# Kernel optimization log

Hardware: AMD Instinct MI355X
Metric: run time of the kernel (lower is better)

Reference implementation:

```python
import jax, jax.numpy as jnp
import numpy as np

EMBED_DIM = 1024
NUM_HEADS = 16
HEAD_DIM = EMBED_DIM // NUM_HEADS


def setup_inputs() -> dict:
    key = jax.random.key(0)
    kx, kq, kk, kv, ko = jax.random.split(key, 5)
    scale = 1.0 / np.sqrt(EMBED_DIM)
    return {
        "x": jax.random.normal(kx, (4, 2048, EMBED_DIM), dtype=jnp.float32),
        # nn.Linear weights are [out, in]; y = x @ W.T
        "w_q": jax.random.normal(kq, (EMBED_DIM, EMBED_DIM), dtype=jnp.float32) * scale,
        "w_k": jax.random.normal(kk, (EMBED_DIM, EMBED_DIM), dtype=jnp.float32) * scale,
        "w_v": jax.random.normal(kv, (EMBED_DIM, EMBED_DIM), dtype=jnp.float32) * scale,
        "w_o": jax.random.normal(ko, (EMBED_DIM, EMBED_DIM), dtype=jnp.float32) * scale,
    }


def reference(x, w_q, w_k, w_v, w_o):
    b, s, _ = x.shape
    # projections (Linear with no bias: x @ W.T)
    q = (x @ w_q.T).reshape(b, s, NUM_HEADS, HEAD_DIM).transpose(0, 2, 1, 3)
    k = (x @ w_k.T).reshape(b, s, NUM_HEADS, HEAD_DIM).transpose(0, 2, 1, 3)
    v = (x @ w_v.T).reshape(b, s, NUM_HEADS, HEAD_DIM).transpose(0, 2, 1, 3)
    # scores: [b, h, s, s]
    scores = jnp.einsum("bhqd,bhkd->bhqk", q, k) / jnp.sqrt(jnp.float32(HEAD_DIM)).astype(x.dtype)
    attn = jax.nn.softmax(scores, axis=-1)
    out = jnp.einsum("bhqk,bhkd->bhqd", attn, v)  # [b, h, s, d]
    out = out.transpose(0, 2, 1, 3).reshape(b, s, EMBED_DIM)
    return out @ w_o.T
```

## Files before the change

### kernel.cpp

```cpp
#include <hip/hip_runtime.h>
#include <math.h>

#define EMBED 1024
#define NHEAD 16
#define HDIM  64
#define BATCH 4
#define SEQ   2048
#define MROWS (BATCH * SEQ)

typedef __attribute__((ext_vector_type(8))) short short8;
typedef __attribute__((ext_vector_type(4))) float floatx4;
typedef __attribute__((ext_vector_type(16))) float floatx16;

#if __has_builtin(__builtin_amdgcn_exp2f)
#define EXP2(x) __builtin_amdgcn_exp2f(x)
#else
#define EXP2(x) exp2f(x)
#endif

__device__ __forceinline__ unsigned short f2bf(float f) {
  unsigned u = __float_as_uint(f);
  u += 0x7fffu + ((u >> 16) & 1u);
  return (unsigned short)(u >> 16);
}

#if __has_builtin(__builtin_amdgcn_cvt_pk_bf16_f32)
__device__ __forceinline__ unsigned pack2bf(float lo, float hi) {
  typedef __attribute__((ext_vector_type(2))) __bf16 bf2;
  union { bf2 b; unsigned u; } c;
  c.b = __builtin_amdgcn_cvt_pk_bf16_f32(lo, hi);
  return c.u;
}
#else
__device__ __forceinline__ unsigned pack2bf(float lo, float hi) {
  return ((__float_as_uint(lo) + 0x8000u) >> 16) |
         ((__float_as_uint(hi) + 0x8000u) & 0xffff0000u);
}
#endif

__device__ __forceinline__ void gl_lds16(const void* g, void* l) {
  __builtin_amdgcn_global_load_lds(
      (const __attribute__((address_space(1))) unsigned int*)g,
      (__attribute__((address_space(3))) unsigned int*)l, 16, 0, 0);
}

__global__ __launch_bounds__(256) void cast_bf16_kernel(
    const float* __restrict__ x,  const float* __restrict__ wq,
    const float* __restrict__ wk, const float* __restrict__ wv,
    const float* __restrict__ wo,
    unsigned short* __restrict__ xb, unsigned short* __restrict__ wb) {
  const size_t NX = (size_t)MROWS * EMBED;
  size_t i4 = ((size_t)blockIdx.x * 256 + threadIdx.x) * 4;
  const float* src;
  unsigned short* dst;
  size_t off;
  if (i4 < NX) {
    src = x; dst = xb; off = i4;
  } else {
    size_t j = i4 - NX;
    int r = (int)(j >> 20);
    off = j & ((1u << 20) - 1);
    src = (r == 0) ? wq : (r == 1) ? wk : (r == 2) ? wv : wo;
    dst = wb + ((size_t)r << 20);
  }
  float4 v = *(const float4*)(src + off);
  ushort4 o;
  o.x = f2bf(v.x); o.y = f2bf(v.y); o.z = f2bf(v.z); o.w = f2bf(v.w);
  *(ushort4*)(dst + off) = o;
}

__device__ __forceinline__ void gemm_core(
    const unsigned short* __restrict__ Amat,
    const unsigned short* __restrict__ Bmat,
    int mBase, int nBase,
    unsigned short* As, unsigned short* Bs,
    floatx4 acc[4][4]) {
  const int t = threadIdx.x;
  const int lane = t & 63, w = t >> 6;
  const int wr = w >> 1, wc = w & 1;
  const int quad = lane >> 4, l15 = lane & 15;

  const int f0 = (w * 2 + 0) * 64 + lane;
  const int f1 = (w * 2 + 1) * 64 + lane;
  const unsigned short* ga0 = Amat + (size_t)(mBase + (f0 >> 2)) * EMBED + (f0 & 3) * 8;
  const unsigned short* ga1 = Amat + (size_t)(mBase + (f1 >> 2)) * EMBED + (f1 & 3) * 8;
  const unsigned short* gb0 = Bmat + (size_t)(nBase + (f0 >> 2)) * EMBED + (f0 & 3) * 8;
  const unsigned short* gb1 = Bmat + (size_t)(nBase + (f1 >> 2)) * EMBED + (f1 & 3) * 8;
  unsigned short* la0 = As + (w * 2 + 0) * 512;
  unsigned short* la1 = As + (w * 2 + 1) * 512;
  unsigned short* lb0 = Bs + (w * 2 + 0) * 512;
  unsigned short* lb1 = Bs + (w * 2 + 1) * 512;

  for (int kb = 0; kb < EMBED; kb += 32) {
    __syncthreads();
    gl_lds16(ga0 + kb, la0);
    gl_lds16(ga1 + kb, la1);
    gl_lds16(gb0 + kb, lb0);
    gl_lds16(gb1 + kb, lb1);
    __syncthreads();
    short8 a[4], b[4];
#pragma unroll
    for (int mi = 0; mi < 4; ++mi)
      a[mi] = *(const short8*)&As[(wr * 64 + mi * 16 + l15) * 32 + quad * 8];
#pragma unroll
    for (int ni = 0; ni < 4; ++ni)
      b[ni] = *(const short8*)&Bs[(wc * 64 + ni * 16 + l15) * 32 + quad * 8];
#pragma unroll
    for (int mi = 0; mi < 4; ++mi)
#pragma unroll
      for (int ni = 0; ni < 4; ++ni)
        acc[mi][ni] = __builtin_amdgcn_mfma_f32_16x16x32_bf16(
            a[mi], b[ni], acc[mi][ni], 0, 0, 0);
  }
}

__global__ __launch_bounds__(256) void proj_qkv_bf16(
    const unsigned short* __restrict__ xb,
    const unsigned short* __restrict__ wb,
    unsigned short* __restrict__ qkv) {
  const int which = blockIdx.z;
  const unsigned short* W = wb + ((size_t)which << 20);
  const int nBase = blockIdx.x * 128;
  const int mBase = blockIdx.y * 128;

  __shared__ unsigned short As[128 * 32];
  __shared__ unsigned short Bs[128 * 32];

  floatx4 acc[4][4] = {};
  gemm_core(xb, W, mBase, nBase, As, Bs, acc);

  const int t = threadIdx.x;
  const int lane = t & 63, w = t >> 6;
  const int wr = w >> 1, wc = w & 1;
  const int quad = lane >> 4, l15 = lane & 15;

  unsigned short* out = qkv + (size_t)which * MROWS * EMBED;
  if (which < 2) {
    const float scale = (which == 0) ? 0.18033688f : 1.0f;
#pragma unroll
    for (int mi = 0; mi < 4; ++mi)
#pragma unroll
      for (int ni = 0; ni < 4; ++ni) {
        const int n = nBase + wc * 64 + ni * 16 + l15;
        const int h = n >> 6, d = n & 63;
#pragma unroll
        for (int r = 0; r < 4; ++r) {
          const int m = mBase + wr * 64 + mi * 16 + quad * 4 + r;
          const int b = m >> 11, s = m & (SEQ - 1);
          out[(((size_t)(b * NHEAD + h) * SEQ) + s) * HDIM + d] =
              f2bf(acc[mi][ni][r] * scale);
        }
      }
  } else {
#pragma unroll
    for (int mi = 0; mi < 4; ++mi) {
      const int m0 = mBase + wr * 64 + mi * 16 + quad * 4;
      const int b = m0 >> 11, s0 = m0 & (SEQ - 1);
#pragma unroll
      for (int ni = 0; ni < 4; ++ni) {
        const int n = nBase + wc * 64 + ni * 16 + l15;
        const int h = n >> 6, d = n & 63;
        ushort4 pk;
        pk.x = f2bf(acc[mi][ni][0]); pk.y = f2bf(acc[mi][ni][1]);
        pk.z = f2bf(acc[mi][ni][2]); pk.w = f2bf(acc[mi][ni][3]);
        *(ushort4*)&out[((size_t)(b * NHEAD + h) * HDIM + d) * SEQ + s0] = pk;
      }
    }
  }
}

__global__ __launch_bounds__(256) void attn_mfma(
    const unsigned short* __restrict__ qkv,
    unsigned short* __restrict__ aout) {
  const unsigned short* Q = qkv;
  const unsigned short* K = qkv + (size_t)MROWS * EMBED;
  const unsigned short* V = qkv + 2 * (size_t)MROWS * EMBED;

  const int id = blockIdx.x;
  const int xcd = id & 7, slot = id >> 3;
  const int bh = xcd * 8 + (slot >> 4);
  const int qBase = (slot & 15) * 128;

  __shared__ unsigned short Ks[2 * 64 * 64];
  __shared__ unsigned short Vs[2 * 64 * 64];

  const int t = threadIdx.x;
  const int lane = t & 63, w = t >> 6;
  const int h2 = lane >> 5;
  const int q31 = lane & 31;

  const unsigned short* qrow =
      Q + ((size_t)bh * SEQ + qBase + w * 32 + q31) * HDIM;
  short8 qa[4];
#pragma unroll
  for (int ds = 0; ds < 4; ++ds)
    qa[ds] = *(const short8*)(qrow + ds * 16 + h2 * 8);

  const int f0 = (w * 2 + 0) * 64 + lane;
  const int f1 = (w * 2 + 1) * 64 + lane;
  const int kr0 = f0 >> 3, kg0 = (f0 & 7) ^ (kr0 & 7);
  const int kr1 = f1 >> 3, kg1 = (f1 & 7) ^ (kr1 & 7);
  const unsigned short* kbase = K + (size_t)bh * SEQ * HDIM;
  const unsigned short* vbase = V + (size_t)bh * HDIM * SEQ;
  const unsigned short* gk0 = kbase + (size_t)kr0 * HDIM + kg0 * 8;
  const unsigned short* gk1 = kbase + (size_t)kr1 * HDIM + kg1 * 8;
  const unsigned short* gv0 = vbase + (size_t)kr0 * SEQ + kg0 * 8;
  const unsigned short* gv1 = vbase + (size_t)kr1 * SEQ + kg1 * 8;
  unsigned short* lk0 = Ks + (w * 2 + 0) * 512;
  unsigned short* lk1 = Ks + (w * 2 + 1) * 512;
  unsigned short* lv0 = Vs + (w * 2 + 0) * 512;
  unsigned short* lv1 = Vs + (w * 2 + 1) * 512;

  floatx16 ot0 = {}, ot1 = {};
  floatx16 osum = {};

  const short one_bf = (short)0x3F80;
  const short8 onesA = {one_bf, one_bf, one_bf, one_bf,
                        one_bf, one_bf, one_bf, one_bf};

  gl_lds16(gk0, lk0);
  gl_lds16(gk1, lk1);
  gl_lds16(gv0, lv0);
  gl_lds16(gv1, lv1);

  for (int kt = 0; kt < SEQ; kt += 64) {
    const int buf = (kt >> 6) & 1;
    const int boff = buf * 4096;
    __syncthreads();
    if (kt + 64 < SEQ) {
      const int noff = (boff ^ 4096);
      gl_lds16(gk0 + (size_t)(kt + 64) * HDIM, lk0 + noff);
      gl_lds16(gk1 + (size_t)(kt + 64) * HDIM, lk1 + noff);
      gl_lds16(gv0 + (kt + 64), lv0 + noff);
      gl_lds16(gv1 + (kt + 64), lv1 + noff);
    }

    floatx16 st0 = {}, st1 = {};
#pragma unroll
    for (int ds = 0; ds < 4; ++ds) {
      const int g = ds * 2 + h2;
      short8 ka0 = *(const short8*)&Ks[boff + q31 * 64 + ((g ^ (q31 & 7)) * 8)];
      st0 = __builtin_amdgcn_mfma_f32_32x32x16_bf16(ka0, qa[ds], st0, 0, 0, 0);
      const int k1 = 32 + q31;
      short8 ka1 = *(const short8*)&Ks[boff + k1 * 64 + ((g ^ (k1 & 7)) * 8)];
      st1 = __builtin_amdgcn_mfma_f32_32x32x16_bf16(ka1, qa[ds], st1, 0, 0, 0);
    }

    unsigned pk0[8], pk1[8], sw0[8], sw1[8];
#pragma unroll
    for (int i = 0; i < 8; ++i) {
      pk0[i] = pack2bf(EXP2(st0[2 * i]), EXP2(st0[2 * i + 1]));
      sw0[i] = __shfl_xor(pk0[i], 32);
      pk1[i] = pack2bf(EXP2(st1[2 * i]), EXP2(st1[2 * i + 1]));
      sw1[i] = __shfl_xor(pk1[i], 32);
    }

#pragma unroll
    for (int kst = 0; kst < 4; ++kst) {
      const unsigned* pk = (kst < 2) ? pk0 : pk1;
      const unsigned* sw = (kst < 2) ? sw0 : sw1;
      const int kl = kst & 1;
      union { unsigned u[4]; short8 s; } pb;
      pb.u[0] = h2 ? sw[4 * kl + 2] : pk[4 * kl + 0];
      pb.u[1] = h2 ? sw[4 * kl + 3] : pk[4 * kl + 1];
      pb.u[2] = h2 ? pk[4 * kl + 2] : sw[4 * kl + 0];
      pb.u[3] = h2 ? pk[4 * kl + 3] : sw[4 * kl + 1];

      osum = __builtin_amdgcn_mfma_f32_32x32x16_bf16(onesA, pb.s, osum, 0, 0, 0);

      const int g = kst * 2 + h2;
      short8 va0 = *(const short8*)&Vs[boff + q31 * 64 + ((g ^ (q31 & 7)) * 8)];
      ot0 = __builtin_amdgcn_mfma_f32_32x32x16_bf16(va0, pb.s, ot0, 0, 0, 0);
      const int d1 = 32 + q31;
      short8 va1 = *(const short8*)&Vs[boff + d1 * 64 + ((g ^ (d1 & 7)) * 8)];
      ot1 = __builtin_amdgcn_mfma_f32_32x32x16_bf16(va1, pb.s, ot1, 0, 0, 0);
    }
  }

  const float inv = 1.0f / osum[0];

  const int b = bh >> 4, hh = bh & 15;
  unsigned short* orow =
      aout + ((size_t)b * SEQ + qBase + w * 32 + q31) * EMBED + hh * HDIM;
#pragma unroll
  for (int rg = 0; rg < 4; ++rg) {
    const int d0 = rg * 8 + h2 * 4;
    ushort4 p0, p1;
    p0.x = f2bf(ot0[4 * rg + 0] * inv); p0.y = f2bf(ot0[4 * rg + 1] * inv);
    p0.z = f2bf(ot0[4 * rg + 2] * inv); p0.w = f2bf(ot0[4 * rg + 3] * inv);
    *(ushort4*)(orow + d0) = p0;
    p1.x = f2bf(ot1[4 * rg + 0] * inv); p1.y = f2bf(ot1[4 * rg + 1] * inv);
    p1.z = f2bf(ot1[4 * rg + 2] * inv); p1.w = f2bf(ot1[4 * rg + 3] * inv);
    *(ushort4*)(orow + 32 + d0) = p1;
  }
}

__global__ __launch_bounds__(256) void out_proj_bf16(
    const unsigned short* __restrict__ aout,
    const unsigned short* __restrict__ wb,
    float* __restrict__ Cout) {
  const int nBase = blockIdx.x * 128;
  const int mBase = blockIdx.y * 128;

  __shared__ unsigned short As[128 * 32];
  __shared__ unsigned short Bs[128 * 32];

  floatx4 acc[4][4] = {};
  gemm_core(aout, wb + ((size_t)3 << 20), mBase, nBase, As, Bs, acc);

  const int t = threadIdx.x;
  const int lane = t & 63, w = t >> 6;
  const int wr = w >> 1, wc = w & 1;
  const int quad = lane >> 4, l15 = lane & 15;

#pragma unroll
  for (int mi = 0; mi < 4; ++mi)
#pragma unroll
    for (int ni = 0; ni < 4; ++ni) {
      const int n = nBase + wc * 64 + ni * 16 + l15;
#pragma unroll
      for (int r = 0; r < 4; ++r) {
        const int m = mBase + wr * 64 + mi * 16 + quad * 4 + r;
        Cout[(size_t)m * EMBED + n] = acc[mi][ni][r];
      }
    }
}

extern "C" void kernel_launch(void* const* d_in, const int* in_sizes, int n_in,
                              void* d_out, int out_size, void* d_ws, size_t ws_size,
                              hipStream_t stream) {
  const float* x  = (const float*)d_in[0];
  const float* wq = (const float*)d_in[1];
  const float* wk = (const float*)d_in[2];
  const float* wv = (const float*)d_in[3];
  const float* wo = (const float*)d_in[4];
  float* out = (float*)d_out;

  char* ws = (char*)d_ws;
  unsigned short* xb   = (unsigned short*)(ws);
  unsigned short* wb   = (unsigned short*)(ws + (16u << 20));
  unsigned short* qkv  = (unsigned short*)(ws + (26u << 20));
  unsigned short* aout = (unsigned short*)(ws + (76u << 20));

  cast_bf16_kernel<<<12288, 256, 0, stream>>>(x, wq, wk, wv, wo, xb, wb);
  proj_qkv_bf16<<<dim3(EMBED / 128, MROWS / 128, 3), 256, 0, stream>>>(xb, wb, qkv);
  attn_mfma<<<1024, 256, 0, stream>>>(qkv, aout);
  out_proj_bf16<<<dim3(EMBED / 128, MROWS / 128), 256, 0, stream>>>(aout, wb, out);
}
```

Measured before the change: 320.9 us.

## Replace double-buffered 64-key tiles with single-buffered 128-key tiles in attention

```diff
diff --git a/kernel.cpp b/kernel.cpp
--- a/kernel.cpp
+++ b/kernel.cpp
@@ -181,8 +181,8 @@
   const int bh = xcd * 8 + (slot >> 4);
   const int qBase = (slot & 15) * 128;
 
-  __shared__ unsigned short Ks[2 * 64 * 64];
-  __shared__ unsigned short Vs[2 * 64 * 64];
+  __shared__ unsigned short Ks[128 * 64];
+  __shared__ unsigned short Vs[64 * 128];
 
   const int t = threadIdx.x;
   const int lane = t & 63, w = t >> 6;
@@ -196,20 +196,22 @@
   for (int ds = 0; ds < 4; ++ds)
     qa[ds] = *(const short8*)(qrow + ds * 16 + h2 * 8);
 
-  const int f0 = (w * 2 + 0) * 64 + lane;
-  const int f1 = (w * 2 + 1) * 64 + lane;
-  const int kr0 = f0 >> 3, kg0 = (f0 & 7) ^ (kr0 & 7);
-  const int kr1 = f1 >> 3, kg1 = (f1 & 7) ^ (kr1 & 7);
   const unsigned short* kbase = K + (size_t)bh * SEQ * HDIM;
   const unsigned short* vbase = V + (size_t)bh * HDIM * SEQ;
-  const unsigned short* gk0 = kbase + (size_t)kr0 * HDIM + kg0 * 8;
-  const unsigned short* gk1 = kbase + (size_t)kr1 * HDIM + kg1 * 8;
-  const unsigned short* gv0 = vbase + (size_t)kr0 * SEQ + kg0 * 8;
-  const unsigned short* gv1 = vbase + (size_t)kr1 * SEQ + kg1 * 8;
-  unsigned short* lk0 = Ks + (w * 2 + 0) * 512;
-  unsigned short* lk1 = Ks + (w * 2 + 1) * 512;
-  unsigned short* lv0 = Vs + (w * 2 + 0) * 512;
-  unsigned short* lv1 = Vs + (w * 2 + 1) * 512;
+  const unsigned short* gk[4];
+  const unsigned short* gv[4];
+  unsigned short* lk[4];
+  unsigned short* lv[4];
+#pragma unroll
+  for (int i = 0; i < 4; ++i) {
+    const int c = (w * 4 + i) * 64 + lane;
+    const int krow = c >> 3, kgrp = (c & 7) ^ (krow & 7);
+    gk[i] = kbase + (size_t)krow * HDIM + kgrp * 8;
+    const int vd = c >> 4, vj = (c & 15) ^ (vd & 15);
+    gv[i] = vbase + (size_t)vd * SEQ + vj * 8;
+    lk[i] = Ks + (w * 4 + i) * 512;
+    lv[i] = Vs + (w * 4 + i) * 512;
+  }
 
   floatx16 ot0 = {}, ot1 = {};
   floatx16 osum = {};
@@ -218,62 +220,60 @@
   const short8 onesA = {one_bf, one_bf, one_bf, one_bf,
                         one_bf, one_bf, one_bf, one_bf};
 
-  gl_lds16(gk0, lk0);
-  gl_lds16(gk1, lk1);
-  gl_lds16(gv0, lv0);
-  gl_lds16(gv1, lv1);
-
-  for (int kt = 0; kt < SEQ; kt += 64) {
-    const int buf = (kt >> 6) & 1;
-    const int boff = buf * 4096;
+  for (int kt = 0; kt < SEQ; kt += 128) {
     __syncthreads();
-    if (kt + 64 < SEQ) {
-      const int noff = (boff ^ 4096);
-      gl_lds16(gk0 + (size_t)(kt + 64) * HDIM, lk0 + noff);
-      gl_lds16(gk1 + (size_t)(kt + 64) * HDIM, lk1 + noff);
-      gl_lds16(gv0 + (kt + 64), lv0 + noff);
-      gl_lds16(gv1 + (kt + 64), lv1 + noff);
+#pragma unroll
+    for (int i = 0; i < 4; ++i) {
+      gl_lds16(gk[i] + (size_t)kt * HDIM, lk[i]);
+      gl_lds16(gv[i] + kt, lv[i]);
     }
-
-    floatx16 st0 = {}, st1 = {};
-#pragma unroll
-    for (int ds = 0; ds < 4; ++ds) {
-      const int g = ds * 2 + h2;
-      short8 ka0 = *(const short8*)&Ks[boff + q31 * 64 + ((g ^ (q31 & 7)) * 8)];
-      st0 = __builtin_amdgcn_mfma_f32_32x32x16_bf16(ka0, qa[ds], st0, 0, 0, 0);
-      const int k1 = 32 + q31;
-      short8 ka1 = *(const short8*)&Ks[boff + k1 * 64 + ((g ^ (k1 & 7)) * 8)];
-      st1 = __builtin_amdgcn_mfma_f32_32x32x16_bf16(ka1, qa[ds], st1, 0, 0, 0);
-    }
-
-    unsigned pk0[8], pk1[8], sw0[8], sw1[8];
-#pragma unroll
-    for (int i = 0; i < 8; ++i) {
-      pk0[i] = pack2bf(EXP2(st0[2 * i]), EXP2(st0[2 * i + 1]));
-      sw0[i] = __shfl_xor(pk0[i], 32);
-      pk1[i] = pack2bf(EXP2(st1[2 * i]), EXP2(st1[2 * i + 1]));
-      sw1[i] = __shfl_xor(pk1[i], 32);
-    }
-
-#pragma unroll
-    for (int kst = 0; kst < 4; ++kst) {
-      const unsigned* pk = (kst < 2) ? pk0 : pk1;
-      const unsigned* sw = (kst < 2) ? sw0 : sw1;
-      const int kl = kst & 1;
-      union { unsigned u[4]; short8 s; } pb;
-      pb.u[0] = h2 ? sw[4 * kl + 2] : pk[4 * kl + 0];
-      pb.u[1] = h2 ? sw[4 * kl + 3] : pk[4 * kl + 1];
-      pb.u[2] = h2 ? pk[4 * kl + 2] : sw[4 * kl + 0];
-      pb.u[3] = h2 ? pk[4 * kl + 3] : sw[4 * kl + 1];
-
-      osum = __builtin_amdgcn_mfma_f32_32x32x16_bf16(onesA, pb.s, osum, 0, 0, 0);
-
-      const int g = kst * 2 + h2;
-      short8 va0 = *(const short8*)&Vs[boff + q31 * 64 + ((g ^ (q31 & 7)) * 8)];
-      ot0 = __builtin_amdgcn_mfma_f32_32x32x16_bf16(va0, pb.s, ot0, 0, 0, 0);
-      const int d1 = 32 + q31;
-      short8 va1 = *(const short8*)&Vs[boff + d1 * 64 + ((g ^ (d1 & 7)) * 8)];
-      ot1 = __builtin_amdgcn_mfma_f32_32x32x16_bf16(va1, pb.s, ot1, 0, 0, 0);
+    __syncthreads();
+
+#pragma unroll
+    for (int sub = 0; sub < 2; ++sub) {
+      const int koff = sub * 64;
+
+      floatx16 st0 = {}, st1 = {};
+#pragma unroll
+      for (int ds = 0; ds < 4; ++ds) {
+        const int g = ds * 2 + h2;
+        const int k0 = koff + q31;
+        short8 ka0 = *(const short8*)&Ks[k0 * 64 + ((g ^ (q31 & 7)) * 8)];
+        st0 = __builtin_amdgcn_mfma_f32_32x32x16_bf16(ka0, qa[ds], st0, 0, 0, 0);
+        const int k1 = koff + 32 + q31;
+        short8 ka1 = *(const short8*)&Ks[k1 * 64 + ((g ^ (q31 & 7)) * 8)];
+        st1 = __builtin_amdgcn_mfma_f32_32x32x16_bf16(ka1, qa[ds], st1, 0, 0, 0);
+      }
+
+      unsigned pk0[8], pk1[8], sw0[8], sw1[8];
+#pragma unroll
+      for (int i = 0; i < 8; ++i) {
+        pk0[i] = pack2bf(EXP2(st0[2 * i]), EXP2(st0[2 * i + 1]));
+        sw0[i] = __shfl_xor(pk0[i], 32);
+        pk1[i] = pack2bf(EXP2(st1[2 * i]), EXP2(st1[2 * i + 1]));
+        sw1[i] = __shfl_xor(pk1[i], 32);
+      }
+
+#pragma unroll
+      for (int kst = 0; kst < 4; ++kst) {
+        const unsigned* pk = (kst < 2) ? pk0 : pk1;
+        const unsigned* sw = (kst < 2) ? sw0 : sw1;
+        const int kl = kst & 1;
+        union { unsigned u[4]; short8 s; } pb;
+        pb.u[0] = h2 ? sw[4 * kl + 2] : pk[4 * kl + 0];
+        pb.u[1] = h2 ? sw[4 * kl + 3] : pk[4 * kl + 1];
+        pb.u[2] = h2 ? pk[4 * kl + 2] : sw[4 * kl + 0];
+        pb.u[3] = h2 ? pk[4 * kl + 3] : sw[4 * kl + 1];
+
+        osum = __builtin_amdgcn_mfma_f32_32x32x16_bf16(onesA, pb.s, osum, 0, 0, 0);
+
+        const int j = sub * 8 + kst * 2 + h2;
+        short8 va0 = *(const short8*)&Vs[q31 * 128 + ((j ^ (q31 & 15)) * 8)];
+        ot0 = __builtin_amdgcn_mfma_f32_32x32x16_bf16(va0, pb.s, ot0, 0, 0, 0);
+        const int d1 = 32 + q31;
+        short8 va1 = *(const short8*)&Vs[d1 * 128 + ((j ^ (d1 & 15)) * 8)];
+        ot1 = __builtin_amdgcn_mfma_f32_32x32x16_bf16(va1, pb.s, ot1, 0, 0, 0);
+      }
     }
   }
 
```

Result: no change. 316.0 us (-1.5%).
